# Kernel tuning notes

Measured on AMD Instinct MI355X. Metric: run time of the kernel, lower is better.

Reference implementation:

```python
import jax, jax.numpy as jnp
import numpy as np

WINDOW = 33  # must match init_kwargs window_size (odd)


def setup_inputs() -> dict:
    key = jax.random.key(0)
    kq, kk, kv, km = jax.random.split(key, 4)
    B, S, D = 4, 2048, 256
    query = jax.random.normal(kq, (B, S, D), dtype=jnp.float32)
    k = jax.random.normal(kk, (B, S, D), dtype=jnp.float32)
    value = jax.random.normal(kv, (B, S, D), dtype=jnp.float32)
    mask = jax.random.randint(km, (B, S), 0, 2).astype(jnp.int32)
    return {"query": query, "key": k, "value": value, "mask": mask}


def reference(query, key, value, mask):
    # Local (sliding-window) attention, window centered at each position.
    B, S, D = query.shape
    half = WINDOW // 2
    offs = jnp.arange(-half, half + 1)                 # [W]
    idx = jnp.arange(S)[:, None] + offs[None, :]       # [S, W]
    valid = (idx >= 0) & (idx < S)                     # in-bounds window entries
    idxc = jnp.clip(idx, 0, S - 1)
    k_win = key[:, idxc]                               # [B, S, W, D]
    v_win = value[:, idxc]                             # [B, S, W, D]
    scores = jnp.einsum('bsd,bswd->bsw', query, k_win) / jnp.sqrt(jnp.float32(D))
    m_win = (mask[:, idxc] != 0) & valid[None]         # [B, S, W]
    scores = jnp.where(m_win, scores, jnp.float32(-1e10))  # masked_fill(-1e10)
    p_attn = jax.nn.softmax(scores, axis=-1)           # [B, S, W]
    values = jnp.einsum('bsw,bswd->bsd', p_attn, v_win)
    return values, p_attn
```

## Files before the change

### kernel.cpp

```cpp
#include <hip/hip_runtime.h>

#define S_LEN 2048
#define D_DIM 256
#define WIN 33
#define HALF 16
#define TROWS 32
#define SPAN 64
#define SC_STRIDE 68
#define PT_STRIDE 72

typedef __attribute__((ext_vector_type(8))) short short8_t;
typedef __attribute__((ext_vector_type(4))) float f32x4;

__device__ inline unsigned short f32_to_bf16(float f) {
    unsigned u = __float_as_uint(f);
    return (unsigned short)((u + 0x7fffu + ((u >> 16) & 1u)) >> 16);
}
__device__ inline unsigned pack2_bf16(float lo, float hi) {
    unsigned a = __float_as_uint(lo) + 0x8000u;
    unsigned b = __float_as_uint(hi) + 0x8000u;
    return __builtin_amdgcn_perm(b, a, 0x07060302);
}
__device__ inline short8_t pack_bf16x8(float4 x, float4 y) {
    union { unsigned u[4]; short8_t s; } r;
    r.u[0] = pack2_bf16(x.x, x.y); r.u[1] = pack2_bf16(x.z, x.w);
    r.u[2] = pack2_bf16(y.x, y.y); r.u[3] = pack2_bf16(y.z, y.w);
    return r.s;
}

__global__ __launch_bounds__(512) void local_attn_v6(
    const float* __restrict__ q,
    const float* __restrict__ k,
    const float* __restrict__ v,
    const int*   __restrict__ mask,
    float* __restrict__ out_v,
    float* __restrict__ out_p)
{
    __shared__ __align__(16) float          Sc[TROWS * SC_STRIDE];
    __shared__ __align__(16) unsigned short Pt[TROWS * PT_STRIDE];
    __shared__ int wm[SPAN];

    const int t    = threadIdx.x;
    const int lane = t & 63;
    const int w    = t >> 6;
    const int l15  = lane & 15;
    const int q4   = lane >> 4;
    const int rt   = w >> 2;
    const int wq   = w & 3;

    const int bid  = blockIdx.x;
    const int tile = ((bid & 7) << 5) | (bid >> 3);
    const int b    = tile >> 6;
    const int s0   = (tile & 63) << 5;

    const float* qb = q + ((size_t)b * S_LEN + s0) * D_DIM;
    const float* kb = k + (size_t)b * S_LEN * D_DIM;
    const float* vb = v + (size_t)b * S_LEN * D_DIM;

    if (t < SPAN) {
        const int idx = s0 - HALF + t;
        wm[t] = (idx >= 0 && idx < S_LEN) ? (mask[b * S_LEN + idx] != 0) : 0;
    }

    {
        const int c    = wq * 16 + l15;
        const int kidx = min(max(s0 - HALF + c, 0), S_LEN - 1);
        const float* kr = kb + (size_t)kidx * D_DIM;
        const float* qr = qb + (size_t)(rt * 16 + l15) * D_DIM;
        f32x4 acc = (f32x4){0.f, 0.f, 0.f, 0.f};
#pragma unroll
        for (int ks = 0; ks < 8; ++ks) {
            const float* pq = qr + ks * 32 + q4 * 8;
            const float* pk = kr + ks * 32 + q4 * 8;
            const short8_t aq = pack_bf16x8(*(const float4*)pq, *(const float4*)(pq + 4));
            const short8_t bk = pack_bf16x8(*(const float4*)pk, *(const float4*)(pk + 4));
            acc = __builtin_amdgcn_mfma_f32_16x16x32_bf16(aq, bk, acc, 0, 0, 0);
        }
#pragma unroll
        for (int r = 0; r < 4; ++r)
            Sc[(rt * 16 + q4 * 4 + r) * SC_STRIDE + c] = acc[r];
    }

    short8_t bv[4][2];
    {
        float vr[4][2][8];
#pragma unroll
        for (int dct = 0; dct < 4; ++dct) {
            const int d = wq * 64 + dct * 16 + l15;
#pragma unroll
            for (int ks = 0; ks < 2; ++ks)
#pragma unroll
                for (int j = 0; j < 8; ++j) {
                    const int g   = ks * 32 + q4 * 8 + j;
                    const int idx = min(max(s0 - HALF + g, 0), S_LEN - 1);
                    vr[dct][ks][j] = vb[(size_t)idx * D_DIM + d];
                }
        }
#pragma unroll
        for (int dct = 0; dct < 4; ++dct)
#pragma unroll
            for (int ks = 0; ks < 2; ++ks) {
                float4 x, y;
                x.x = vr[dct][ks][0]; x.y = vr[dct][ks][1];
                x.z = vr[dct][ks][2]; x.w = vr[dct][ks][3];
                y.x = vr[dct][ks][4]; y.y = vr[dct][ks][5];
                y.z = vr[dct][ks][6]; y.w = vr[dct][ks][7];
                bv[dct][ks] = pack_bf16x8(x, y);
            }
    }
    __syncthreads();

    {
        const int row = t >> 4;
        const int e   = t & 15;
        const float4 s4 = *(const float4*)&Sc[row * SC_STRIDE + 4 * e];
        const float sarr[4] = {s4.x, s4.y, s4.z, s4.w};
        float vs[4];
#pragma unroll
        for (int kq = 0; kq < 4; ++kq) {
            const int c = 4 * e + kq;
            const int j = c - row;
            const bool inb = (j >= 0) && (j < WIN);
            vs[kq] = inb ? (wm[c] ? sarr[kq] * 0.0625f : -1e10f) : -1e30f;
        }
        float m = fmaxf(fmaxf(vs[0], vs[1]), fmaxf(vs[2], vs[3]));
        m = fmaxf(m, __shfl_xor(m, 1, 64));
        m = fmaxf(m, __shfl_xor(m, 2, 64));
        m = fmaxf(m, __shfl_xor(m, 4, 64));
        m = fmaxf(m, __shfl_xor(m, 8, 64));
        float s = 0.f;
#pragma unroll
        for (int kq = 0; kq < 4; ++kq) { vs[kq] = __expf(vs[kq] - m); s += vs[kq]; }
        s += __shfl_xor(s, 1, 64);
        s += __shfl_xor(s, 2, 64);
        s += __shfl_xor(s, 4, 64);
        s += __shfl_xor(s, 8, 64);
        const float rinv = 1.0f / s;

        float ps[4];
        union { unsigned short u[4]; uint2 d2; } pw;
#pragma unroll
        for (int kq = 0; kq < 4; ++kq) {
            ps[kq]   = vs[kq] * rinv;
            pw.u[kq] = f32_to_bf16(ps[kq]);
        }
        *(uint2*)&Pt[row * PT_STRIDE + 4 * e] = pw.d2;
        float* prow = out_p + ((size_t)(b * S_LEN + s0 + row)) * WIN;
#pragma unroll
        for (int kq = 0; kq < 4; ++kq) {
            const int j = 4 * e + kq - row;
            if (j >= 0 && j < WIN) prow[j] = ps[kq];
        }
    }
    __syncthreads();

    {
        const short8_t ap0 = *(const short8_t*)&Pt[(rt * 16 + l15) * PT_STRIDE + q4 * 8];
        const short8_t ap1 = *(const short8_t*)&Pt[(rt * 16 + l15) * PT_STRIDE + 32 + q4 * 8];
        float* ob = out_v + ((size_t)b * S_LEN + s0) * D_DIM;
#pragma unroll
        for (int dct = 0; dct < 4; ++dct) {
            f32x4 acc = (f32x4){0.f, 0.f, 0.f, 0.f};
            acc = __builtin_amdgcn_mfma_f32_16x16x32_bf16(ap0, bv[dct][0], acc, 0, 0, 0);
            acc = __builtin_amdgcn_mfma_f32_16x16x32_bf16(ap1, bv[dct][1], acc, 0, 0, 0);
            const int d = wq * 64 + dct * 16 + l15;
#pragma unroll
            for (int r = 0; r < 4; ++r)
                ob[(size_t)(rt * 16 + q4 * 4 + r) * D_DIM + d] = acc[r];
        }
    }
}

extern "C" void kernel_launch(void* const* d_in, const int* in_sizes, int n_in,
                              void* d_out, int out_size, void* d_ws, size_t ws_size,
                              hipStream_t stream) {
    const float* q    = (const float*)d_in[0];
    const float* k    = (const float*)d_in[1];
    const float* v    = (const float*)d_in[2];
    const int*   mask = (const int*)d_in[3];

    const int B = 4;
    float* out_v = (float*)d_out;
    float* out_p = (float*)d_out + (size_t)B * S_LEN * D_DIM;

    const int blocks = B * (S_LEN / TROWS);
    local_attn_v6<<<blocks, 512, 0, stream>>>(q, k, v, mask, out_v, out_p);
}
```

Before: 83.53 us.

## Halve row tile to 16 rows and remap waves over head dimension

Processes 16 query rows per block instead of 32, doubling the grid, and redistributes waves so three compute the QK scores and all eight split the value dimension for PV. Softmax now uses 32 threads per row over a 48-key span, and the second PV k-slice is zero-padded. This aims to raise parallelism and cut per-block register pressure, at the cost of more redundant halo loads of K and V per output row.

```diff
diff --git a/kernel.cpp b/kernel.cpp
--- a/kernel.cpp
+++ b/kernel.cpp
@@ -4,8 +4,8 @@
 #define D_DIM 256
 #define WIN 33
 #define HALF 16
-#define TROWS 32
-#define SPAN 64
+#define TROWS 16
+#define SPAN 48
 #define SC_STRIDE 68
 #define PT_STRIDE 72
 
@@ -28,7 +28,7 @@
     return r.s;
 }
 
-__global__ __launch_bounds__(512) void local_attn_v6(
+__global__ __launch_bounds__(512) void local_attn_v7(
     const float* __restrict__ q,
     const float* __restrict__ k,
     const float* __restrict__ v,
@@ -45,13 +45,11 @@
     const int w    = t >> 6;
     const int l15  = lane & 15;
     const int q4   = lane >> 4;
-    const int rt   = w >> 2;
-    const int wq   = w & 3;
 
     const int bid  = blockIdx.x;
-    const int tile = ((bid & 7) << 5) | (bid >> 3);
-    const int b    = tile >> 6;
-    const int s0   = (tile & 63) << 5;
+    const int tile = ((bid & 7) << 6) | (bid >> 3);
+    const int b    = tile >> 7;
+    const int s0   = (tile & 127) << 4;
 
     const float* qb = q + ((size_t)b * S_LEN + s0) * D_DIM;
     const float* kb = k + (size_t)b * S_LEN * D_DIM;
@@ -62,11 +60,11 @@
         wm[t] = (idx >= 0 && idx < S_LEN) ? (mask[b * S_LEN + idx] != 0) : 0;
     }
 
-    {
-        const int c    = wq * 16 + l15;
+    if (w < 3) {
+        const int c    = 16 * w + l15;
         const int kidx = min(max(s0 - HALF + c, 0), S_LEN - 1);
         const float* kr = kb + (size_t)kidx * D_DIM;
-        const float* qr = qb + (size_t)(rt * 16 + l15) * D_DIM;
+        const float* qr = qb + (size_t)l15 * D_DIM;
         f32x4 acc = (f32x4){0.f, 0.f, 0.f, 0.f};
 #pragma unroll
         for (int ks = 0; ks < 8; ++ks) {
@@ -78,95 +76,100 @@
         }
 #pragma unroll
         for (int r = 0; r < 4; ++r)
-            Sc[(rt * 16 + q4 * 4 + r) * SC_STRIDE + c] = acc[r];
+            Sc[(q4 * 4 + r) * SC_STRIDE + c] = acc[r];
     }
 
-    short8_t bv[4][2];
+    short8_t bv[2][2];
     {
-        float vr[4][2][8];
+        const bool act1 = (q4 < 2);
+        const short8_t zfrag = {0,0,0,0,0,0,0,0};
+        float vr[2][2][8];
 #pragma unroll
-        for (int dct = 0; dct < 4; ++dct) {
-            const int d = wq * 64 + dct * 16 + l15;
+        for (int nt = 0; nt < 2; ++nt) {
+            const int d = 32 * w + nt * 16 + l15;
 #pragma unroll
-            for (int ks = 0; ks < 2; ++ks)
+            for (int j = 0; j < 8; ++j) {
+                const int g0   = q4 * 8 + j;
+                const int idx0 = min(max(s0 - HALF + g0, 0), S_LEN - 1);
+                vr[nt][0][j] = vb[(size_t)idx0 * D_DIM + d];
+            }
+            if (act1) {
 #pragma unroll
                 for (int j = 0; j < 8; ++j) {
-                    const int g   = ks * 32 + q4 * 8 + j;
-                    const int idx = min(max(s0 - HALF + g, 0), S_LEN - 1);
-                    vr[dct][ks][j] = vb[(size_t)idx * D_DIM + d];
+                    const int g1   = 32 + q4 * 8 + j;
+                    const int idx1 = min(max(s0 - HALF + g1, 0), S_LEN - 1);
+                    vr[nt][1][j] = vb[(size_t)idx1 * D_DIM + d];
                 }
+            }
         }
 #pragma unroll
-        for (int dct = 0; dct < 4; ++dct)
-#pragma unroll
-            for (int ks = 0; ks < 2; ++ks) {
-                float4 x, y;
-                x.x = vr[dct][ks][0]; x.y = vr[dct][ks][1];
-                x.z = vr[dct][ks][2]; x.w = vr[dct][ks][3];
-                y.x = vr[dct][ks][4]; y.y = vr[dct][ks][5];
-                y.z = vr[dct][ks][6]; y.w = vr[dct][ks][7];
-                bv[dct][ks] = pack_bf16x8(x, y);
+        for (int nt = 0; nt < 2; ++nt) {
+            float4 x, y;
+            x.x = vr[nt][0][0]; x.y = vr[nt][0][1]; x.z = vr[nt][0][2]; x.w = vr[nt][0][3];
+            y.x = vr[nt][0][4]; y.y = vr[nt][0][5]; y.z = vr[nt][0][6]; y.w = vr[nt][0][7];
+            bv[nt][0] = pack_bf16x8(x, y);
+            if (act1) {
+                x.x = vr[nt][1][0]; x.y = vr[nt][1][1]; x.z = vr[nt][1][2]; x.w = vr[nt][1][3];
+                y.x = vr[nt][1][4]; y.y = vr[nt][1][5]; y.z = vr[nt][1][6]; y.w = vr[nt][1][7];
+                bv[nt][1] = pack_bf16x8(x, y);
+            } else {
+                bv[nt][1] = zfrag;
             }
-    }
-    __syncthreads();
-
-    {
-        const int row = t >> 4;
-        const int e   = t & 15;
-        const float4 s4 = *(const float4*)&Sc[row * SC_STRIDE + 4 * e];
-        const float sarr[4] = {s4.x, s4.y, s4.z, s4.w};
-        float vs[4];
-#pragma unroll
-        for (int kq = 0; kq < 4; ++kq) {
-            const int c = 4 * e + kq;
-            const int j = c - row;
-            const bool inb = (j >= 0) && (j < WIN);
-            vs[kq] = inb ? (wm[c] ? sarr[kq] * 0.0625f : -1e10f) : -1e30f;
-        }
-        float m = fmaxf(fmaxf(vs[0], vs[1]), fmaxf(vs[2], vs[3]));
-        m = fmaxf(m, __shfl_xor(m, 1, 64));
-        m = fmaxf(m, __shfl_xor(m, 2, 64));
-        m = fmaxf(m, __shfl_xor(m, 4, 64));
-        m = fmaxf(m, __shfl_xor(m, 8, 64));
-        float s = 0.f;
-#pragma unroll
-        for (int kq = 0; kq < 4; ++kq) { vs[kq] = __expf(vs[kq] - m); s += vs[kq]; }
-        s += __shfl_xor(s, 1, 64);
-        s += __shfl_xor(s, 2, 64);
-        s += __shfl_xor(s, 4, 64);
-        s += __shfl_xor(s, 8, 64);
-        const float rinv = 1.0f / s;
-
-        float ps[4];
-        union { unsigned short u[4]; uint2 d2; } pw;
-#pragma unroll
-        for (int kq = 0; kq < 4; ++kq) {
-            ps[kq]   = vs[kq] * rinv;
-            pw.u[kq] = f32_to_bf16(ps[kq]);
-        }
-        *(uint2*)&Pt[row * PT_STRIDE + 4 * e] = pw.d2;
-        float* prow = out_p + ((size_t)(b * S_LEN + s0 + row)) * WIN;
-#pragma unroll
-        for (int kq = 0; kq < 4; ++kq) {
-            const int j = 4 * e + kq - row;
-            if (j >= 0 && j < WIN) prow[j] = ps[kq];
         }
     }
     __syncthreads();
 
     {
-        const short8_t ap0 = *(const short8_t*)&Pt[(rt * 16 + l15) * PT_STRIDE + q4 * 8];
-        const short8_t ap1 = *(const short8_t*)&Pt[(rt * 16 + l15) * PT_STRIDE + 32 + q4 * 8];
+        const int row = t >> 5;
+        const int e   = t & 31;
+        float vs[2];
+#pragma unroll
+        for (int kq = 0; kq < 2; ++kq) {
+            const int c = 2 * e + kq;
+            const int j = c - row;
+            const bool inb = (j >= 0) && (j < WIN) && (c < SPAN);
+            vs[kq] = inb ? (wm[c < SPAN ? c : 0] ? Sc[row * SC_STRIDE + (c < SPAN ? c : 0)] * 0.0625f
+                                                 : -1e10f)
+                         : -1e30f;
+        }
+        float m = fmaxf(vs[0], vs[1]);
+        m = fmaxf(m, __shfl_xor(m, 1, 64));
+        m = fmaxf(m, __shfl_xor(m, 2, 64));
+        m = fmaxf(m, __shfl_xor(m, 4, 64));
+        m = fmaxf(m, __shfl_xor(m, 8, 64));
+        m = fmaxf(m, __shfl_xor(m, 16, 64));
+        float s = 0.f;
+#pragma unroll
+        for (int kq = 0; kq < 2; ++kq) { vs[kq] = __expf(vs[kq] - m); s += vs[kq]; }
+        s += __shfl_xor(s, 1, 64);
+        s += __shfl_xor(s, 2, 64);
+        s += __shfl_xor(s, 4, 64);
+        s += __shfl_xor(s, 8, 64);
+        s += __shfl_xor(s, 16, 64);
+        const float rinv = 1.0f / s;
+
+        float p0 = vs[0] * rinv, p1 = vs[1] * rinv;
+        *(unsigned*)&Pt[row * PT_STRIDE + 2 * e] = pack2_bf16(p0, p1);
+        float* prow = out_p + ((size_t)(b * S_LEN + s0 + row)) * WIN;
+        const int j0 = 2 * e - row;
+        if (j0 >= 0 && j0 < WIN)     prow[j0]     = p0;
+        if (j0 + 1 >= 0 && j0 + 1 < WIN) prow[j0 + 1] = p1;
+    }
+    __syncthreads();
+
+    {
+        const short8_t ap0 = *(const short8_t*)&Pt[l15 * PT_STRIDE + q4 * 8];
+        const short8_t ap1 = *(const short8_t*)&Pt[l15 * PT_STRIDE + 32 + q4 * 8];
         float* ob = out_v + ((size_t)b * S_LEN + s0) * D_DIM;
 #pragma unroll
-        for (int dct = 0; dct < 4; ++dct) {
+        for (int nt = 0; nt < 2; ++nt) {
             f32x4 acc = (f32x4){0.f, 0.f, 0.f, 0.f};
-            acc = __builtin_amdgcn_mfma_f32_16x16x32_bf16(ap0, bv[dct][0], acc, 0, 0, 0);
-            acc = __builtin_amdgcn_mfma_f32_16x16x32_bf16(ap1, bv[dct][1], acc, 0, 0, 0);
-            const int d = wq * 64 + dct * 16 + l15;
+            acc = __builtin_amdgcn_mfma_f32_16x16x32_bf16(ap0, bv[nt][0], acc, 0, 0, 0);
+            acc = __builtin_amdgcn_mfma_f32_16x16x32_bf16(ap1, bv[nt][1], acc, 0, 0, 0);
+            const int d = 32 * w + nt * 16 + l15;
 #pragma unroll
             for (int r = 0; r < 4; ++r)
-                ob[(size_t)(rt * 16 + q4 * 4 + r) * D_DIM + d] = acc[r];
+                ob[(size_t)(q4 * 4 + r) * D_DIM + d] = acc[r];
         }
     }
 }
@@ -184,5 +187,5 @@
     float* out_p = (float*)d_out + (size_t)B * S_LEN * D_DIM;
 
     const int blocks = B * (S_LEN / TROWS);
-    local_attn_v6<<<blocks, 512, 0, stream>>>(q, k, v, mask, out_v, out_p);
+    local_attn_v7<<<blocks, 512, 0, stream>>>(q, k, v, mask, out_v, out_p);
 }
```

Measured after the change: 83.25 us. About the same (-0.3%).
